# Kernel optimization log

Hardware: AMD Instinct MI355X
Metric: run time of the kernel (lower is better)

The kernel has to match this reference:

```python
import jax, jax.numpy as jnp
import numpy as np

D_MODEL = 2048
D_INNER = 4096   # expand * d_model == ngroups * d_state
D_XB = 1024
N_HEADS = 32     # = ngroups
HEAD_DIM = 128   # = d_state
N_KV_HEADS = D_XB // HEAD_DIM  # 8
N_REP = N_HEADS // N_KV_HEADS  # 4
D_IN_PROJ = D_INNER + 2 * D_XB + D_INNER + N_HEADS  # 10272
ROPE_BASE = 10000.0


def setup_inputs() -> dict:
    key = jax.random.key(0)
    k1, k2, k3 = jax.random.split(key, 3)
    u = jax.random.normal(k1, (2, 2048, D_MODEL), dtype=jnp.float32)
    W_in = jax.random.normal(k2, (D_IN_PROJ, D_MODEL), dtype=jnp.float32) * (1.0 / np.sqrt(D_MODEL))
    W_out = jax.random.normal(k3, (D_MODEL, D_INNER), dtype=jnp.float32) * (1.0 / np.sqrt(D_INNER))
    return {"u": u, "W_in": W_in, "W_out": W_out}


def _rotate_half(x):
    x1, x2 = jnp.split(x, 2, axis=-1)
    return jnp.concatenate((-x2, x1), axis=-1)


def _rope_cos_sin(seqlen, dim, dtype):
    inv_freq = 1.0 / (ROPE_BASE ** (jnp.arange(0, dim, 2, dtype=jnp.float32) / dim))
    pos = jnp.arange(seqlen, dtype=jnp.float32)
    freqs = pos[:, None] * inv_freq[None, :]          # [S, dim/2]
    emb = jnp.concatenate((freqs, freqs), axis=-1)    # [S, dim]
    return jnp.cos(emb).astype(dtype), jnp.sin(emb).astype(dtype)


def reference(u, W_in, W_out):
    # NOTE: the module's forward short-circuits (early return) into a GQA
    # attention path; the SSM code after the return is dead.
    B, S, _ = u.shape
    zxbcdt = jnp.einsum('bsd,ed->bse', u, W_in)       # [B, S, D_IN_PROJ]
    # split: z (d_inner), x (d_xb), B (d_xb), C (d_inner), dt (nheads); d_mlp = 0
    o0 = D_INNER
    x = zxbcdt[..., o0:o0 + D_XB]
    Bm = zxbcdt[..., o0 + D_XB:o0 + 2 * D_XB]
    C = zxbcdt[..., o0 + 2 * D_XB:o0 + 2 * D_XB + D_INNER]
    # q = C (32 heads), k = B (8 heads), v = x (8 heads); [B, H, S, Dh]
    q = C.reshape(B, S, N_HEADS, HEAD_DIM).transpose(0, 2, 1, 3)
    k = Bm.reshape(B, S, N_KV_HEADS, HEAD_DIM).transpose(0, 2, 1, 3)
    v = x.reshape(B, S, N_KV_HEADS, HEAD_DIM).transpose(0, 2, 1, 3)
    cos, sin = _rope_cos_sin(S, HEAD_DIM, u.dtype)    # [S, Dh]
    cos = cos[None, None]                             # [1, 1, S, Dh]
    sin = sin[None, None]
    q = q * cos + _rotate_half(q) * sin
    k = k * cos + _rotate_half(k) * sin
    # repeat_kv: repeat_interleave along head dim
    k = jnp.repeat(k, N_REP, axis=1)
    v = jnp.repeat(v, N_REP, axis=1)
    scale = 1.0 / np.sqrt(HEAD_DIM)
    scores = jnp.einsum('bhqd,bhkd->bhqk', q, k) * scale
    causal = jnp.tril(jnp.ones((S, S), dtype=bool))
    scores = jnp.where(causal[None, None], scores, jnp.finfo(scores.dtype).min)
    attn = jax.nn.softmax(scores, axis=-1)
    out = jnp.einsum('bhqk,bhkd->bhqd', attn, v)      # [B, H, S, Dh]
    out = out.transpose(0, 2, 1, 3).reshape(B, S, D_INNER)
    return jnp.einsum('bse,de->bsd', out, W_out)      # [B, S, d_model]
```

## Files before the change

### kernel.cpp

```cpp
#include <hip/hip_runtime.h>
#include <stdint.h>

#define S_LEN 2048
#define BATCH 2
#define NH 32
#define NKV 8
#define HD 128
#define NE 6144

typedef __attribute__((ext_vector_type(8))) short short8;
typedef __attribute__((ext_vector_type(4))) float floatx4;

__device__ __forceinline__ unsigned short f2bf(float f) {
    union { float f; uint32_t u; } v; v.f = f;
    uint32_t u = v.u;
    u += 0x7FFFu + ((u >> 16) & 1u);
    return (unsigned short)(u >> 16);
}
__device__ __forceinline__ float bf2f(unsigned short h) {
    union { uint32_t u; float f; } v; v.u = ((uint32_t)h) << 16;
    return v.f;
}

__global__ void cast_f32_bf16(const float* __restrict__ in,
                              unsigned short* __restrict__ out, int n4) {
    int i = blockIdx.x * blockDim.x + threadIdx.x;
    if (i >= n4) return;
    float4 f = reinterpret_cast<const float4*>(in)[i];
    ushort4 o;
    o.x = f2bf(f.x); o.y = f2bf(f.y); o.z = f2bf(f.z); o.w = f2bf(f.w);
    reinterpret_cast<ushort4*>(out)[i] = o;
}

template <int OUT_BF16>
__global__ void __launch_bounds__(256)
gemm_bt(const unsigned short* __restrict__ A, const unsigned short* __restrict__ Bt,
        void* __restrict__ Cv, int M, int N, int K) {
    __shared__ unsigned short As[128 * 32];
    __shared__ unsigned short Bs[128 * 32];
    const int tid  = threadIdx.x;
    const int w    = tid >> 6;
    const int lane = tid & 63;
    const int quad = lane >> 4;
    const int l16  = lane & 15;
    const int wm   = w >> 1, wn = w & 1;
    const int m0 = blockIdx.y * 128, n0 = blockIdx.x * 128;

    floatx4 acc[4][4];
#pragma unroll
    for (int i = 0; i < 4; i++)
#pragma unroll
        for (int j = 0; j < 4; j++) acc[i][j] = {0.f, 0.f, 0.f, 0.f};

    const int lr = lane >> 2;
    const int lk = (lane & 3) * 8;
    const int KT = K >> 5;

    for (int kt = 0; kt < KT; ++kt) {
        const int k0 = kt << 5;
        __syncthreads();
#pragma unroll
        for (int c = 0; c < 2; ++c) {
            const int chunk = w * 2 + c;
            const unsigned short* ga = A  + (size_t)(m0 + chunk * 16 + lr) * K + k0 + lk;
            __builtin_amdgcn_global_load_lds(
                (const __attribute__((address_space(1))) void*)ga,
                (__attribute__((address_space(3))) void*)(As + chunk * 512), 16, 0, 0);
            const unsigned short* gb = Bt + (size_t)(n0 + chunk * 16 + lr) * K + k0 + lk;
            __builtin_amdgcn_global_load_lds(
                (const __attribute__((address_space(1))) void*)gb,
                (__attribute__((address_space(3))) void*)(Bs + chunk * 512), 16, 0, 0);
        }
        __syncthreads();
        short8 af[4], bf[4];
#pragma unroll
        for (int t = 0; t < 4; ++t) {
            af[t] = *reinterpret_cast<const short8*>(As + (wm * 64 + t * 16 + l16) * 32 + quad * 8);
            bf[t] = *reinterpret_cast<const short8*>(Bs + (wn * 64 + t * 16 + l16) * 32 + quad * 8);
        }
#pragma unroll
        for (int i = 0; i < 4; i++)
#pragma unroll
            for (int j = 0; j < 4; j++)
                acc[i][j] = __builtin_amdgcn_mfma_f32_16x16x32_bf16(af[i], bf[j], acc[i][j], 0, 0, 0);
    }

#pragma unroll
    for (int i = 0; i < 4; i++)
#pragma unroll
        for (int j = 0; j < 4; j++) {
            const int row = m0 + wm * 64 + i * 16 + quad * 4;
            const int col = n0 + wn * 64 + j * 16 + l16;
#pragma unroll
            for (int r = 0; r < 4; r++) {
                float vv = acc[i][j][r];
                if (OUT_BF16)
                    ((unsigned short*)Cv)[(size_t)(row + r) * N + col] = f2bf(vv);
                else
                    ((float*)Cv)[(size_t)(row + r) * N + col] = vv;
            }
        }
}

#define QSCALE 0.12748539509360f
__global__ void rope_split(const unsigned short* __restrict__ Z,
                           unsigned short* __restrict__ Q,
                           unsigned short* __restrict__ Kb,
                           unsigned short* __restrict__ Vt) {
    const int PER_TOK = 2048 + 512 + 1024;
    int idx = blockIdx.x * blockDim.x + threadIdx.x;
    if (idx >= BATCH * S_LEN * PER_TOK) return;
    int t = idx / PER_TOK;
    int r = idx - t * PER_TOK;
    int b = t / S_LEN, s = t - b * S_LEN;
    const unsigned short* z = Z + (size_t)t * NE;
    if (r < 2048) {
        int h = r >> 6, j = r & 63;
        float x0 = bf2f(z[2048 + h * 128 + j]);
        float x1 = bf2f(z[2048 + h * 128 + j + 64]);
        float inv = exp2f((float)j * -0.20762050593f);
        float c, sn; sincosf((float)s * inv, &sn, &c);
        size_t base = ((size_t)(b * NH + h) * S_LEN + s) * HD;
        Q[base + j]      = f2bf((x0 * c - x1 * sn) * QSCALE);
        Q[base + j + 64] = f2bf((x1 * c + x0 * sn) * QSCALE);
    } else if (r < 2560) {
        int rr = r - 2048; int kh = rr >> 6, j = rr & 63;
        float x0 = bf2f(z[1024 + kh * 128 + j]);
        float x1 = bf2f(z[1024 + kh * 128 + j + 64]);
        float inv = exp2f((float)j * -0.20762050593f);
        float c, sn; sincosf((float)s * inv, &sn, &c);
        size_t base = ((size_t)(b * NKV + kh) * S_LEN + s) * HD;
        Kb[base + j]      = f2bf(x0 * c - x1 * sn);
        Kb[base + j + 64] = f2bf(x1 * c + x0 * sn);
    } else {
        int m = r - 2560; int kh = m >> 7, d = m & 127;
        Vt[((size_t)(b * NKV + kh) * HD + d) * S_LEN + s] = z[m];
    }
}

__global__ void __launch_bounds__(256)
attn_kernel(const unsigned short* __restrict__ Q,
            const unsigned short* __restrict__ Kb,
            const unsigned short* __restrict__ Vt,
            unsigned short* __restrict__ Ob) {
    __shared__ unsigned short Ks[2][64 * 128];
    __shared__ unsigned short Vs[2][64 * 128];
    __shared__ unsigned short Ps[4][16 * 72];
    const int tid  = threadIdx.x;
    const int w    = tid >> 6;
    const int lane = tid & 63;
    const int quad = lane >> 4;
    const int l16  = lane & 15;
    const int blk = blockIdx.x;
    const int qt = 31 - (blk >> 6);
    const int bh = blk & 63;
    const int h = bh & 31, b = bh >> 5;
    const int kvh = h >> 2;
    const int qw0 = qt * 64 + w * 16;

    const unsigned short* Qbase = Q  + ((size_t)(b * NH  + h)   * S_LEN) * HD;
    const unsigned short* Kbase = Kb + ((size_t)(b * NKV + kvh) * S_LEN) * HD;
    const unsigned short* Vbase = Vt + ((size_t)(b * NKV + kvh) * HD) * S_LEN;

    short8 qf[4];
    {
        const unsigned short* qrow = Qbase + (size_t)(qw0 + l16) * HD + quad * 8;
#pragma unroll
        for (int ks = 0; ks < 4; ++ks)
            qf[ks] = *reinterpret_cast<const short8*>(qrow + ks * 32);
    }

    floatx4 oacc[8];
#pragma unroll
    for (int i = 0; i < 8; i++) oacc[i] = {0.f, 0.f, 0.f, 0.f};
    float lsum[4] = {0.f, 0.f, 0.f, 0.f};

    const unsigned short* kp[4];
    const unsigned short* vp[4];
#pragma unroll
    for (int c = 0; c < 4; ++c) {
        const int bI = w * 4 + c;
        const int krow = bI * 4 + (lane >> 4);
        kp[c] = Kbase + (size_t)krow * HD + ((lane & 15) ^ (krow & 7)) * 8;
        const int drow = bI * 8 + (lane >> 3);
        vp[c] = Vbase + (size_t)drow * S_LEN + ((lane & 7) ^ (drow & 7)) * 8;
    }

    const int NT = qt + 1;

#define STAGE(BUF) do {                                                        \
    unsigned short* kd = &Ks[BUF][0];                                          \
    unsigned short* vd = &Vs[BUF][0];                                          \
    _Pragma("unroll")                                                          \
    for (int c = 0; c < 4; ++c) {                                              \
        const int bI = w * 4 + c;                                              \
        __builtin_amdgcn_global_load_lds(                                      \
            (const __attribute__((address_space(1))) void*)kp[c],              \
            (__attribute__((address_space(3))) void*)(kd + bI * 512), 16, 0, 0);\
        __builtin_amdgcn_global_load_lds(                                      \
            (const __attribute__((address_space(1))) void*)vp[c],              \
            (__attribute__((address_space(3))) void*)(vd + bI * 512), 16, 0, 0);\
        kp[c] += 64 * HD; vp[c] += 64;                                         \
    }                                                                          \
} while (0)

    STAGE(0);
    asm volatile("s_waitcnt vmcnt(0)" ::: "memory");
    __builtin_amdgcn_s_barrier();
    asm volatile("" ::: "memory");

    unsigned short* pw  = &Ps[w][0];
    unsigned short* pst = pw + quad * 288 + l16;
    const unsigned short* prd = pw + l16 * 72 + quad * 8;

    int cur = 0;
    for (int t = 0; t < NT; ++t) {
        if (t + 1 < NT) STAGE(cur ^ 1);

        const bool diag = (t == qt);
        const int kv0 = t << 6;
        const unsigned short* Kc = &Ks[cur][0];
        const unsigned short* Vc = &Vs[cur][0];

        floatx4 sacc[4];
#pragma unroll
        for (int nb = 0; nb < 4; nb++) sacc[nb] = {0.f, 0.f, 0.f, 0.f};
        __builtin_amdgcn_s_setprio(1);
#pragma unroll
        for (int ks = 0; ks < 4; ++ks) {
#pragma unroll
            for (int nb = 0; nb < 4; ++nb) {
                const int srow = nb * 16 + l16;
                const int pc = (ks * 4 + quad) ^ (l16 & 7);
                short8 kf = *reinterpret_cast<const short8*>(Kc + srow * 128 + pc * 8);
                sacc[nb] = __builtin_amdgcn_mfma_f32_16x16x32_bf16(qf[ks], kf, sacc[nb], 0, 0, 0);
            }
        }
        __builtin_amdgcn_s_setprio(0);

#pragma unroll
        for (int nb = 0; nb < 4; ++nb) {
            const int col = kv0 + nb * 16 + l16;
#pragma unroll
            for (int r = 0; r < 4; ++r) {
                const int row = qw0 + quad * 4 + r;
                float p = (!diag || col <= row) ? exp2f(sacc[nb][r]) : 0.0f;
                lsum[r] += p;
                pst[r * 72 + nb * 16] = f2bf(p);
            }
        }

        __builtin_amdgcn_s_setprio(1);
#pragma unroll
        for (int kv_sub = 0; kv_sub < 2; ++kv_sub) {
            short8 pf = *reinterpret_cast<const short8*>(prd + kv_sub * 32);
#pragma unroll
            for (int dt = 0; dt < 8; ++dt) {
                const int drow = dt * 16 + l16;
                const int pcV = (kv_sub * 4 + quad) ^ (l16 & 7);
                short8 vf = *reinterpret_cast<const short8*>(Vc + drow * 64 + pcV * 8);
                oacc[dt] = __builtin_amdgcn_mfma_f32_16x16x32_bf16(pf, vf, oacc[dt], 0, 0, 0);
            }
        }
        __builtin_amdgcn_s_setprio(0);

        asm volatile("s_waitcnt vmcnt(0)" ::: "memory");
        __builtin_amdgcn_s_barrier();
        asm volatile("" ::: "memory");
        cur ^= 1;
    }
#undef STAGE

    float linv[4];
#pragma unroll
    for (int r = 0; r < 4; ++r) {
        float s = lsum[r];
#pragma unroll
        for (int off = 1; off < 16; off <<= 1) s += __shfl_xor(s, off);
        linv[r] = 1.0f / s;
    }
#pragma unroll
    for (int dt = 0; dt < 8; ++dt) {
        const int d = dt * 16 + l16;
#pragma unroll
        for (int r = 0; r < 4; ++r) {
            const int row = qw0 + quad * 4 + r;
            Ob[((size_t)(b * S_LEN + row)) * 4096 + h * 128 + d] = f2bf(oacc[dt][r] * linv[r]);
        }
    }
}

extern "C" void kernel_launch(void* const* d_in, const int* in_sizes, int n_in,
                              void* d_out, int out_size, void* d_ws, size_t ws_size,
                              hipStream_t stream) {
    const float* u     = (const float*)d_in[0];
    const float* W_in  = (const float*)d_in[1];
    const float* W_out = (const float*)d_in[2];
    float* out = (float*)d_out;

    char* ws = (char*)d_ws;
    unsigned short* u_bf    = (unsigned short*)(ws);
    unsigned short* win_bf  = (unsigned short*)(ws + 16777216);
    unsigned short* wout_bf = (unsigned short*)(ws + 41943040);
    unsigned short* Z       = (unsigned short*)(ws + 58720256);
    unsigned short* Qb      = (unsigned short*)(ws + 109051904);
    unsigned short* Kv      = (unsigned short*)(ws + 142606336);
    unsigned short* Vt      = (unsigned short*)(ws + 150994944);
    unsigned short* Ob      = (unsigned short*)(ws + 159383552);

    {
        int n4 = (2 * 2048 * 2048) / 4;
        cast_f32_bf16<<<(n4 + 255) / 256, 256, 0, stream>>>(u, u_bf, n4);
        n4 = (6144 * 2048) / 4;
        cast_f32_bf16<<<(n4 + 255) / 256, 256, 0, stream>>>(W_in + (size_t)4096 * 2048, win_bf, n4);
        n4 = (2048 * 4096) / 4;
        cast_f32_bf16<<<(n4 + 255) / 256, 256, 0, stream>>>(W_out, wout_bf, n4);
    }
    {
        dim3 g(6144 / 128, 4096 / 128);
        gemm_bt<1><<<g, 256, 0, stream>>>(u_bf, win_bf, Z, 4096, 6144, 2048);
    }
    {
        int n = BATCH * S_LEN * 3584;
        rope_split<<<(n + 255) / 256, 256, 0, stream>>>(Z, Qb, Kv, Vt);
    }
    attn_kernel<<<BATCH * NH * (S_LEN / 64), 256, 0, stream>>>(Qb, Kv, Vt, Ob);
    {
        dim3 g(2048 / 128, 4096 / 128);
        gemm_bt<0><<<g, 256, 0, stream>>>(Ob, wout_bf, out, 4096, 2048, 4096);
    }
}
```

Baseline: 560.2 us.

## Single-buffer attention K/V tiles, pack P with cvt_pk, permute V layout

Drops the double-buffered K/V LDS staging for a single buffer with barriers around each load, and adds launch_bounds occupancy 4 so more blocks fit per CU. It also permutes the V-transpose layout so packed bf16 pairs of P can be written with v_cvt_pk_bf16_f32 into a swizzled 64-wide P buffer, and splits the diagonal tile into a templated masked path so the non-diagonal tiles skip the mask. In exchange, loads no longer overlap compute within a block, and the design relies on other resident blocks to hide that memory latency.

```diff
diff --git a/kernel.cpp b/kernel.cpp
--- a/kernel.cpp
+++ b/kernel.cpp
@@ -20,6 +20,11 @@
 __device__ __forceinline__ float bf2f(unsigned short h) {
     union { uint32_t u; float f; } v; v.u = ((uint32_t)h) << 16;
     return v.f;
+}
+__device__ __forceinline__ uint32_t cvt_pk_bf16(float lo, float hi) {
+    uint32_t r;
+    asm("v_cvt_pk_bf16_f32 %0, %1, %2" : "=v"(r) : "v"(lo), "v"(hi));
+    return r;
 }
 
 __global__ void cast_f32_bf16(const float* __restrict__ in,
@@ -134,18 +139,85 @@
         Kb[base + j + 64] = f2bf(x1 * c + x0 * sn);
     } else {
         int m = r - 2560; int kh = m >> 7, d = m & 127;
-        Vt[((size_t)(b * NKV + kh) * HD + d) * S_LEN + s] = z[m];
-    }
-}
-
-__global__ void __launch_bounds__(256)
+        int k = s & 63;
+        int kp = (k & 32) + ((k & 15) << 1) + ((k >> 4) & 1);
+        int sp = (s & ~63) | kp;
+        Vt[((size_t)(b * NKV + kh) * HD + d) * S_LEN + sp] = z[m];
+    }
+}
+
+template <bool DIAG>
+__device__ __forceinline__ void attn_tile(
+    const short8 (&qf)[4], floatx4 (&oacc)[8], float (&lsum)[4],
+    const unsigned short* __restrict__ Ks, const unsigned short* __restrict__ Vs,
+    unsigned short* __restrict__ pw, int w, int quad, int l16) {
+    const int e = l16 & 7;
+
+    floatx4 sacc[4];
+#pragma unroll
+    for (int nb = 0; nb < 4; nb++) sacc[nb] = {0.f, 0.f, 0.f, 0.f};
+    __builtin_amdgcn_s_setprio(1);
+#pragma unroll
+    for (int ks = 0; ks < 4; ++ks) {
+#pragma unroll
+        for (int nb = 0; nb < 4; ++nb) {
+            const int srow = nb * 16 + l16;
+            const int pc = (ks * 4 + quad) ^ e;
+            short8 kf = *reinterpret_cast<const short8*>(Ks + srow * 128 + pc * 8);
+            sacc[nb] = __builtin_amdgcn_mfma_f32_16x16x32_bf16(qf[ks], kf, sacc[nb], 0, 0, 0);
+        }
+    }
+    __builtin_amdgcn_s_setprio(0);
+
+    float pv[4][4];
+#pragma unroll
+    for (int nb = 0; nb < 4; ++nb)
+#pragma unroll
+        for (int r = 0; r < 4; ++r) {
+            float p = exp2f(sacc[nb][r]);
+            if (DIAG)
+                p = (nb * 16 + l16 <= w * 16 + quad * 4 + r) ? p : 0.0f;
+            pv[nb][r] = p;
+            lsum[r] += p;
+        }
+
+    const int row0 = quad * 4;
+    const int sub = l16 >> 2, off = (l16 & 3) * 2;
+#pragma unroll
+    for (int r = 0; r < 4; ++r) {
+        const int rowe = (row0 + r) & 7;
+#pragma unroll
+        for (int g = 0; g < 2; ++g) {
+            uint32_t pk = cvt_pk_bf16(pv[g * 2][r], pv[g * 2 + 1][r]);
+            const int chunk = (g * 4 + sub) ^ rowe;
+            *reinterpret_cast<uint32_t*>(pw + (row0 + r) * 64 + chunk * 8 + off) = pk;
+        }
+    }
+
+    __builtin_amdgcn_s_setprio(1);
+#pragma unroll
+    for (int kv_sub = 0; kv_sub < 2; ++kv_sub) {
+        const int pcP = (kv_sub * 4 + quad) ^ e;
+        short8 pf = *reinterpret_cast<const short8*>(pw + l16 * 64 + pcP * 8);
+#pragma unroll
+        for (int dt = 0; dt < 8; ++dt) {
+            const int drow = dt * 16 + l16;
+            const int pcV = (kv_sub * 4 + quad) ^ e;
+            short8 vf = *reinterpret_cast<const short8*>(Vs + drow * 64 + pcV * 8);
+            oacc[dt] = __builtin_amdgcn_mfma_f32_16x16x32_bf16(pf, vf, oacc[dt], 0, 0, 0);
+        }
+    }
+    __builtin_amdgcn_s_setprio(0);
+}
+
+__global__ void __launch_bounds__(256, 4)
 attn_kernel(const unsigned short* __restrict__ Q,
             const unsigned short* __restrict__ Kb,
             const unsigned short* __restrict__ Vt,
             unsigned short* __restrict__ Ob) {
-    __shared__ unsigned short Ks[2][64 * 128];
-    __shared__ unsigned short Vs[2][64 * 128];
-    __shared__ unsigned short Ps[4][16 * 72];
+    __shared__ unsigned short Ks[64 * 128];
+    __shared__ unsigned short Vs[128 * 64];
+    __shared__ unsigned short Ps[4][16 * 64];
     const int tid  = threadIdx.x;
     const int w    = tid >> 6;
     const int lane = tid & 63;
@@ -186,89 +258,32 @@
         vp[c] = Vbase + (size_t)drow * S_LEN + ((lane & 7) ^ (drow & 7)) * 8;
     }
 
-    const int NT = qt + 1;
-
-#define STAGE(BUF) do {                                                        \
-    unsigned short* kd = &Ks[BUF][0];                                          \
-    unsigned short* vd = &Vs[BUF][0];                                          \
+#define STAGE() do {                                                           \
     _Pragma("unroll")                                                          \
     for (int c = 0; c < 4; ++c) {                                              \
         const int bI = w * 4 + c;                                              \
         __builtin_amdgcn_global_load_lds(                                      \
             (const __attribute__((address_space(1))) void*)kp[c],              \
-            (__attribute__((address_space(3))) void*)(kd + bI * 512), 16, 0, 0);\
+            (__attribute__((address_space(3))) void*)(Ks + bI * 512), 16, 0, 0);\
         __builtin_amdgcn_global_load_lds(                                      \
             (const __attribute__((address_space(1))) void*)vp[c],              \
-            (__attribute__((address_space(3))) void*)(vd + bI * 512), 16, 0, 0);\
+            (__attribute__((address_space(3))) void*)(Vs + bI * 512), 16, 0, 0);\
         kp[c] += 64 * HD; vp[c] += 64;                                         \
     }                                                                          \
 } while (0)
 
-    STAGE(0);
-    asm volatile("s_waitcnt vmcnt(0)" ::: "memory");
-    __builtin_amdgcn_s_barrier();
-    asm volatile("" ::: "memory");
-
-    unsigned short* pw  = &Ps[w][0];
-    unsigned short* pst = pw + quad * 288 + l16;
-    const unsigned short* prd = pw + l16 * 72 + quad * 8;
-
-    int cur = 0;
-    for (int t = 0; t < NT; ++t) {
-        if (t + 1 < NT) STAGE(cur ^ 1);
-
-        const bool diag = (t == qt);
-        const int kv0 = t << 6;
-        const unsigned short* Kc = &Ks[cur][0];
-        const unsigned short* Vc = &Vs[cur][0];
-
-        floatx4 sacc[4];
-#pragma unroll
-        for (int nb = 0; nb < 4; nb++) sacc[nb] = {0.f, 0.f, 0.f, 0.f};
-        __builtin_amdgcn_s_setprio(1);
-#pragma unroll
-        for (int ks = 0; ks < 4; ++ks) {
-#pragma unroll
-            for (int nb = 0; nb < 4; ++nb) {
-                const int srow = nb * 16 + l16;
-                const int pc = (ks * 4 + quad) ^ (l16 & 7);
-                short8 kf = *reinterpret_cast<const short8*>(Kc + srow * 128 + pc * 8);
-                sacc[nb] = __builtin_amdgcn_mfma_f32_16x16x32_bf16(qf[ks], kf, sacc[nb], 0, 0, 0);
-            }
-        }
-        __builtin_amdgcn_s_setprio(0);
-
-#pragma unroll
-        for (int nb = 0; nb < 4; ++nb) {
-            const int col = kv0 + nb * 16 + l16;
-#pragma unroll
-            for (int r = 0; r < 4; ++r) {
-                const int row = qw0 + quad * 4 + r;
-                float p = (!diag || col <= row) ? exp2f(sacc[nb][r]) : 0.0f;
-                lsum[r] += p;
-                pst[r * 72 + nb * 16] = f2bf(p);
-            }
-        }
-
-        __builtin_amdgcn_s_setprio(1);
-#pragma unroll
-        for (int kv_sub = 0; kv_sub < 2; ++kv_sub) {
-            short8 pf = *reinterpret_cast<const short8*>(prd + kv_sub * 32);
-#pragma unroll
-            for (int dt = 0; dt < 8; ++dt) {
-                const int drow = dt * 16 + l16;
-                const int pcV = (kv_sub * 4 + quad) ^ (l16 & 7);
-                short8 vf = *reinterpret_cast<const short8*>(Vc + drow * 64 + pcV * 8);
-                oacc[dt] = __builtin_amdgcn_mfma_f32_16x16x32_bf16(pf, vf, oacc[dt], 0, 0, 0);
-            }
-        }
-        __builtin_amdgcn_s_setprio(0);
-
-        asm volatile("s_waitcnt vmcnt(0)" ::: "memory");
-        __builtin_amdgcn_s_barrier();
-        asm volatile("" ::: "memory");
-        cur ^= 1;
-    }
+    unsigned short* pw = &Ps[w][0];
+
+    for (int t = 0; t < qt; ++t) {
+        __syncthreads();
+        STAGE();
+        __syncthreads();
+        attn_tile<false>(qf, oacc, lsum, Ks, Vs, pw, w, quad, l16);
+    }
+    __syncthreads();
+    STAGE();
+    __syncthreads();
+    attn_tile<true>(qf, oacc, lsum, Ks, Vs, pw, w, quad, l16);
 #undef STAGE
 
     float linv[4];
@@ -327,6 +342,6 @@
     attn_kernel<<<BATCH * NH * (S_LEN / 64), 256, 0, stream>>>(Qb, Kv, Vt, Ob);
     {
         dim3 g(2048 / 128, 4096 / 128);
-        gemm_bt<0><<<g, 256, 0, stream>>>(Ob, wout_bf, out, 4096, 2048, 4096);
-    }
-}
+        gemm_bt<0><<<g, 256, 0, stream>>>(Ob, wout_bf, out, 2048 == 2048 ? 4096 : 4096, 2048, 4096);
+    }
+}
```

After: 549.2 us. 2.0% less time.
